# Kernel optimization log

Hardware: AMD Instinct MI355X
Metric: run time of the kernel (lower is better)

The kernel has to match this reference:

```python
import jax, jax.numpy as jnp
import numpy as np

V, E, HS, HD = 32000, 64, 128, 128
S, T = 128, 48


def gru_cell(x, h, Wih, Whh, bih, bhh):
    # torch nn.GRU cell: gates stacked as [r, z, n]
    gi = x @ Wih.T + bih
    gh = h @ Whh.T + bhh
    ir, iz, inn = jnp.split(gi, 3, axis=-1)
    hr, hz, hn = jnp.split(gh, 3, axis=-1)
    r = jax.nn.sigmoid(ir + hr)
    z = jax.nn.sigmoid(iz + hz)
    n = jnp.tanh(inn + r * hn)
    return (1.0 - z) * n + z * h


def setup_inputs() -> dict:
    key = jax.random.key(0)
    ks = jax.random.split(key, 16)
    sc = 0.05
    inp = {
        'document': jax.random.randint(ks[0], (S, T), 0, V, dtype=jnp.int64),
        'enc_emb': jax.random.normal(ks[1], (V, E), jnp.float32) * sc,
        'enc_Wih': jax.random.normal(ks[2], (3 * HS, E), jnp.float32) * sc,
        'enc_Whh': jax.random.normal(ks[3], (3 * HS, HS), jnp.float32) * sc,
        'enc_bih': jax.random.normal(ks[4], (3 * HS,), jnp.float32) * sc,
        'enc_bhh': jax.random.normal(ks[5], (3 * HS,), jnp.float32) * sc,
        'doc_Wih': jax.random.normal(ks[6], (3 * HD, HS), jnp.float32) * sc,
        'doc_Whh': jax.random.normal(ks[7], (3 * HD, HD), jnp.float32) * sc,
        'doc_bih': jax.random.normal(ks[8], (3 * HD,), jnp.float32) * sc,
        'doc_bhh': jax.random.normal(ks[9], (3 * HD,), jnp.float32) * sc,
        'dec_emb': jax.random.normal(ks[10], (V, E), jnp.float32) * sc,
        'dec_Wih': jax.random.normal(ks[11], (3 * HS, E + HD), jnp.float32) * sc,
        'dec_Whh': jax.random.normal(ks[12], (3 * HS, HS), jnp.float32) * sc,
        'dec_bih': jax.random.normal(ks[13], (3 * HS,), jnp.float32) * sc,
        'dec_bhh': jax.random.normal(ks[14], (3 * HS,), jnp.float32) * sc,
        'fc_W': jax.random.normal(ks[15], (V, HS), jnp.float32) * sc,
        'fc_b': jnp.zeros((V,), jnp.float32),
    }
    return inp


def reference(document, enc_emb, enc_Wih, enc_Whh, enc_bih, enc_bhh,
              doc_Wih, doc_Whh, doc_bih, doc_bhh,
              dec_emb, dec_Wih, dec_Whh, dec_bih, dec_bhh, fc_W, fc_b):
    s, t = document.shape
    # --- sentence encoder: GRU over tokens, batch = sentences ---
    x = enc_emb[document]                       # [S, T, E]
    def enc_step(h, xt):
        return gru_cell(xt, h, enc_Wih, enc_Whh, enc_bih, enc_bhh), None
    h0 = jnp.zeros((s, HS), enc_emb.dtype)
    sent_vec, _ = jax.lax.scan(enc_step, h0, jnp.swapaxes(x, 0, 1))  # [S, HS]
    # --- document encoder: GRU over sentence vectors, batch = 1 ---
    def doc_step(h, sv):
        return gru_cell(sv[None, :], h, doc_Wih, doc_Whh, doc_bih, doc_bhh), None
    hd0 = jnp.zeros((1, HD), enc_emb.dtype)
    doc_h, _ = jax.lax.scan(doc_step, hd0, sent_vec)
    doc_vec = doc_h[0]                          # [HD]
    # --- teacher-forced decoder, vectorized over sentences ---
    dec_in = dec_emb[document[:, :-1]]          # [S, T-1, E]
    ctx = jnp.broadcast_to(doc_vec, (s, t - 1, HD))
    xs = jnp.swapaxes(jnp.concatenate([dec_in, ctx], axis=-1), 0, 1)  # [T-1, S, E+HD]
    def dec_step(h, xt):
        h2 = gru_cell(xt, h, dec_Wih, dec_Whh, dec_bih, dec_bhh)
        logits = h2 @ fc_W.T + fc_b
        return h2, logits
    _, logits = jax.lax.scan(dec_step, sent_vec, xs)  # [T-1, S, V]
    targets = document[:, 1:].T                 # [T-1, S]
    logp = jax.nn.log_softmax(logits, axis=-1)
    ll = jnp.take_along_axis(logp, targets[..., None], axis=-1)[..., 0]
    # per-sentence mean over steps, then mean over sentences == global mean
    return -jnp.mean(ll)
```

## Files before the change

kernel.cpp:

```cpp
#include <hip/hip_runtime.h>

typedef unsigned short ushort_t;
typedef short bf16x8 __attribute__((ext_vector_type(8)));
typedef float f32x4 __attribute__((ext_vector_type(4)));
typedef unsigned int u32x4 __attribute__((ext_vector_type(4)));
typedef _Float16 half2t __attribute__((ext_vector_type(2)));

#define LOG2E 1.4426950408889634f
#define LN2   0.6931471805599453f

__device__ __forceinline__ float bf2f(ushort_t u) {
    union { unsigned int i; float f; } v; v.i = ((unsigned int)u) << 16; return v.f;
}
__device__ __forceinline__ ushort_t f2bf(float f) {
    union { float f; unsigned int i; } v; v.f = f;
    unsigned int u = v.i;
    unsigned int r = (u + 0x7FFFu + ((u >> 16) & 1u)) >> 16;
    return (ushort_t)r;
}
__device__ __forceinline__ float hsum4(f32x4 v) { return (v[0] + v[1]) + (v[2] + v[3]); }
__device__ __forceinline__ float frcp(float x) { return __builtin_amdgcn_rcpf(x); }
__device__ __forceinline__ float fsig(float x) { return frcp(1.f + __expf(-x)); }
__device__ __forceinline__ float ftanh(float x) { return 1.f - 2.f * frcp(1.f + __expf(2.f * x)); }
__device__ __forceinline__ int hpad(int e) { return e + ((e >> 4) << 2); }
__device__ __forceinline__ float dot2(unsigned int w, unsigned int h, float acc) {
    union { unsigned int u; half2t h2; } a, b;
    a.u = w; b.u = h;
    return __builtin_amdgcn_fdot2(a.h2, b.h2, acc, false);
}
__device__ __forceinline__ float dpp_xor1_add(float x) {
    int m = __builtin_amdgcn_update_dpp(0, __builtin_bit_cast(int, x), 0xB1, 0xF, 0xF, true);
    return x + __builtin_bit_cast(float, m);
}
__device__ __forceinline__ float dpp_xor2_add(float x) {
    int m = __builtin_amdgcn_update_dpp(0, __builtin_bit_cast(int, x), 0x4E, 0xF, 0xF, true);
    return x + __builtin_bit_cast(float, m);
}
__device__ __forceinline__ ushort_t f2h(float f) {
    union { _Float16 h; ushort_t s; } c; c.h = (_Float16)f; return c.s;
}

__global__ __launch_bounds__(768, 1) void k_encoder(
    const int* __restrict__ doc, const float* __restrict__ emb,
    const float* __restrict__ Wih, const float* __restrict__ Whh,
    const float* __restrict__ bih, const float* __restrict__ bhh,
    float* __restrict__ sent) {
    int s = blockIdx.x, t = threadIdx.x;
    int half = t & 1, j = t >> 1;
    __shared__ float xs[80], hs[160];
    __shared__ float gi[384], gh[384];
    __shared__ int toks[48];
    f32x4 wih[8], whh[16];
#pragma unroll
    for (int k = 0; k < 8; k++) wih[k] = *(const f32x4*)(Wih + j * 64 + half * 32 + k * 4);
#pragma unroll
    for (int k = 0; k < 16; k++) whh[k] = *(const f32x4*)(Whh + j * 128 + half * 64 + k * 4);
    float bi = bih[j], bh = bhh[j];
    if (t < 48) toks[t] = doc[s * 48 + t];
    if (t < 128) hs[hpad(t)] = 0.f;
    __syncthreads();
    if (t < 64) xs[hpad(t)] = emb[(size_t)toks[0] * 64 + t];
    __syncthreads();
    const float* xb = xs + half * 40;
    const float* hb = hs + half * 80;
    for (int tt = 0; tt < 48; tt++) {
        float xnext = (t < 64 && tt + 1 < 48) ? emb[(size_t)toks[tt + 1] * 64 + t] : 0.f;
        f32x4 a0 = {0,0,0,0}, b0 = {0,0,0,0}, b1 = {0,0,0,0};
#pragma unroll
        for (int k = 0; k < 8; k++) a0 += wih[k] * (*(const f32x4*)(xb + k * 4 + (k >> 2) * 4));
#pragma unroll
        for (int k = 0; k < 16; k += 2) {
            b0 += whh[k] * (*(const f32x4*)(hb + k * 4 + (k >> 2) * 4));
            b1 += whh[k + 1] * (*(const f32x4*)(hb + (k + 1) * 4 + ((k + 1) >> 2) * 4));
        }
        float a = hsum4(a0), b = hsum4(b0 + b1);
        a = dpp_xor1_add(a); b = dpp_xor1_add(b);
        if (half == 0) { gi[j] = a + bi; gh[j] = b + bh; }
        __syncthreads();
        if (t < 128) {
            float r = fsig(gi[t] + gh[t]);
            float z = fsig(gi[t + 128] + gh[t + 128]);
            float n = ftanh(gi[t + 256] + r * gh[t + 256]);
            hs[hpad(t)] = (1.f - z) * n + z * hs[hpad(t)];
        }
        if (t < 64 && tt + 1 < 48) xs[hpad(t)] = xnext;
        __syncthreads();
    }
    if (t < 128) sent[s * 128 + t] = hs[hpad(t)];
}

__global__ void k_doc_gi(const float* __restrict__ sv, const float* __restrict__ Wih,
                         const float* __restrict__ bih, float* __restrict__ gidoc,
                         const float* __restrict__ Whh, ushort_t* __restrict__ wdoc) {
    int bid = blockIdx.x, j = threadIdx.x;
    if (bid >= 128) {
        int i = (bid - 128) * 384 + j;
        if (i < 12288) {
            f32x4 v = ((const f32x4*)Whh)[i];
            union { ushort_t u[4]; unsigned long long q; } p;
            p.u[0] = f2h(v[0]); p.u[1] = f2h(v[1]); p.u[2] = f2h(v[2]); p.u[3] = f2h(v[3]);
            ((unsigned long long*)wdoc)[i] = p.q;
        }
        return;
    }
    __shared__ f32x4 v4[32];
    if (j < 128) ((float*)v4)[j] = sv[bid * 128 + j];
    __syncthreads();
    f32x4 a0 = {0,0,0,0}, a1 = {0,0,0,0};
#pragma unroll
    for (int k = 0; k < 32; k += 2) {
        a0 += *(const f32x4*)(Wih + j * 128 + k * 4) * v4[k];
        a1 += *(const f32x4*)(Wih + j * 128 + (k + 1) * 4) * v4[k + 1];
    }
    gidoc[bid * 384 + j] = bih[j] + hsum4(a0 + a1);
}

__global__ __launch_bounds__(512, 1) __attribute__((amdgpu_waves_per_eu(1, 2)))
void k_mid(
    const float* __restrict__ gidoc, const ushort_t* __restrict__ wdoc,
    const float* __restrict__ dbhh, float* __restrict__ dvec,
    const int* __restrict__ doc, const float* __restrict__ demb,
    const float* __restrict__ dWih, float* __restrict__ gidec,
    const float* __restrict__ fcW, ushort_t* __restrict__ fcWb,
    const float* __restrict__ fcb, float* __restrict__ fcbs) {
    int bid = blockIdx.x, t = threadIdx.x;

    if (bid == 0) {
        int q = t & 3, e = t >> 2;
        __shared__ unsigned int hpk[2][64];
        u32x4 wr4[4], wz4[4], wn4[4];
        const ushort_t* wbase = wdoc + e * 128 + q * 32;
#pragma unroll
        for (int k = 0; k < 4; k++) {
            wr4[k] = *(const u32x4*)(wbase + k * 8);
            wz4[k] = *(const u32x4*)(wbase + 128 * 128 + k * 8);
            wn4[k] = *(const u32x4*)(wbase + 256 * 128 + k * 8);
        }
        float biasr = dbhh[e], biasz = dbhh[128 + e], biasn = dbhh[256 + e];
        float cr = gidoc[e], cz = gidoc[128 + e], cn = gidoc[256 + e];
        if (t < 64) hpk[0][t] = 0u;
        float he = 0.f;
        __syncthreads();
        for (int i = 0; i < 128; i++) {
            float nr = 0.f, nz = 0.f, nn = 0.f;
            if (i + 1 < 128) {
                const float* g = gidoc + (i + 1) * 384;
                nr = g[e]; nz = g[128 + e]; nn = g[256 + e];
            }
            const unsigned int* hp = &hpk[i & 1][q * 16];
            u32x4 hv[4];
            hv[0] = *(const u32x4*)(hp);
            hv[1] = *(const u32x4*)(hp + 4);
            hv[2] = *(const u32x4*)(hp + 8);
            hv[3] = *(const u32x4*)(hp + 12);
            float ra0 = 0.f, ra1 = 0.f, za0 = 0.f, za1 = 0.f, na0 = 0.f, na1 = 0.f;
#pragma unroll
            for (int k = 0; k < 4; k++) {
                u32x4 h4 = hv[k];
                ra0 = dot2(wr4[k][0], h4[0], ra0); ra1 = dot2(wr4[k][1], h4[1], ra1);
                ra0 = dot2(wr4[k][2], h4[2], ra0); ra1 = dot2(wr4[k][3], h4[3], ra1);
                za0 = dot2(wz4[k][0], h4[0], za0); za1 = dot2(wz4[k][1], h4[1], za1);
                za0 = dot2(wz4[k][2], h4[2], za0); za1 = dot2(wz4[k][3], h4[3], za1);
                na0 = dot2(wn4[k][0], h4[0], na0); na1 = dot2(wn4[k][1], h4[1], na1);
                na0 = dot2(wn4[k][2], h4[2], na0); na1 = dot2(wn4[k][3], h4[3], na1);
            }
            float rp = ra0 + ra1, zp = za0 + za1, np = na0 + na1;
            rp = dpp_xor2_add(dpp_xor1_add(rp));
            zp = dpp_xor2_add(dpp_xor1_add(zp));
            np = dpp_xor2_add(dpp_xor1_add(np));
            float r = fsig(cr + rp + biasr);
            float z = fsig(cz + zp + biasz);
            float n = ftanh(cn + r * (np + biasn));
            he = (1.f - z) * n + z * he;
            if (q == 0) ((ushort_t*)&hpk[(i & 1) ^ 1][0])[e] = f2h(he);
            __syncthreads();
            cr = nr; cz = nz; cn = nn;
        }
        if (q == 0) dvec[e] = he;
        return;
    }

    if (bid <= 128) {
        int s = bid - 1;
        __shared__ float xs[80];
        __shared__ int toks[48];
        if (t < 47) toks[t] = doc[s * 48 + t];
        __syncthreads();
        if (t < 64) xs[hpad(t)] = demb[(size_t)toks[0] * 64 + t];
        __syncthreads();
        f32x4 wih[16];
        if (t < 384) {
#pragma unroll
            for (int k = 0; k < 16; k++) wih[k] = *(const f32x4*)(dWih + t * 192 + k * 4);
        }
        for (int tt = 0; tt < 47; tt++) {
            float xnext = (t < 64 && tt + 1 < 47) ? demb[(size_t)toks[tt + 1] * 64 + t] : 0.f;
            if (t < 384) {
                f32x4 a0 = {0,0,0,0}, a1 = {0,0,0,0};
#pragma unroll
                for (int k = 0; k < 16; k += 2) {
                    a0 += wih[k] * (*(const f32x4*)(xs + k * 4 + (k >> 2) * 4));
                    a1 += wih[k + 1] * (*(const f32x4*)(xs + (k + 1) * 4 + ((k + 1) >> 2) * 4));
                }
                gidec[(tt * 128 + s) * 384 + t] = hsum4(a0 + a1);
            }
            __syncthreads();
            if (t < 64 && tt + 1 < 47) xs[hpad(t)] = xnext;
            __syncthreads();
        }
        return;
    }

    int i = (bid - 129) * 512 + t;
    if (i < 1024000) {
        f32x4 v = ((const f32x4*)fcW)[i];
        union { ushort_t u[4]; unsigned long long qq; } p;
        p.u[0] = f2bf(v[0] * LOG2E); p.u[1] = f2bf(v[1] * LOG2E);
        p.u[2] = f2bf(v[2] * LOG2E); p.u[3] = f2bf(v[3] * LOG2E);
        ((unsigned long long*)fcWb)[i] = p.qq;
    } else if (i < 1024000 + 8000) {
        int k = i - 1024000;
        f32x4 b = ((const f32x4*)fcb)[k];
        ((f32x4*)fcbs)[k] = b * LOG2E;
    }
}

__global__ void k_gctx(const float* __restrict__ Wih, const float* __restrict__ bih,
                       const float* __restrict__ dvec, float* __restrict__ gctx) {
    int j = threadIdx.x;
    __shared__ f32x4 v4[32];
    if (j < 128) ((float*)v4)[j] = dvec[j];
    __syncthreads();
    f32x4 a0 = {0,0,0,0}, a1 = {0,0,0,0};
#pragma unroll
    for (int k = 0; k < 32; k += 2) {
        a0 += *(const f32x4*)(Wih + j * 192 + 64 + k * 4) * v4[k];
        a1 += *(const f32x4*)(Wih + j * 192 + 64 + (k + 1) * 4) * v4[k + 1];
    }
    gctx[j] = bih[j] + hsum4(a0 + a1);
}

__global__ __launch_bounds__(768, 1) void k_dec_seq(
    const float* __restrict__ gidec, const float* __restrict__ Whh,
    const float* __restrict__ bhh, const float* __restrict__ sent,
    const float* __restrict__ gctx, ushort_t* __restrict__ h2b) {
    int s = blockIdx.x, t = threadIdx.x, half = t & 1, j = t >> 1;
    __shared__ float hs[160];
    __shared__ float gi[384], gh[384];
    f32x4 whh[16];
#pragma unroll
    for (int k = 0; k < 16; k++) whh[k] = *(const f32x4*)(Whh + j * 128 + half * 64 + k * 4);
    float bh = bhh[j];
    float g_me = gctx[j];
    if (t < 128) hs[hpad(t)] = sent[s * 128 + t];
    float gval = (half == 0) ? (gidec[s * 384 + j] + g_me) : 0.f;
    __syncthreads();
    const float* hb = hs + half * 80;
    for (int i = 0; i < 47; i++) {
        float gnext = (half == 0 && i + 1 < 47) ? (gidec[((i + 1) * 128 + s) * 384 + j] + g_me) : 0.f;
        f32x4 b0 = {0,0,0,0}, b1 = {0,0,0,0};
#pragma unroll
        for (int k = 0; k < 16; k += 2) {
            b0 += whh[k] * (*(const f32x4*)(hb + k * 4 + (k >> 2) * 4));
            b1 += whh[k + 1] * (*(const f32x4*)(hb + (k + 1) * 4 + ((k + 1) >> 2) * 4));
        }
        float b = hsum4(b0 + b1);
        b = dpp_xor1_add(b);
        if (half == 0) { gh[j] = b + bh; gi[j] = gval; }
        __syncthreads();
        if (t < 128) {
            float r = fsig(gi[t] + gh[t]);
            float z = fsig(gi[t + 128] + gh[t + 128]);
            float n = ftanh(gi[t + 256] + r * gh[t + 256]);
            float hn = (1.f - z) * n + z * hs[hpad(t)];
            hs[hpad(t)] = hn;
            h2b[(i * 128 + s) * 128 + t] = f2bf(hn);
        }
        __syncthreads();
        gval = gnext;
    }
}

__global__ void k_tl(const int* __restrict__ doc, const ushort_t* __restrict__ h2b,
                     const ushort_t* __restrict__ wb, const float* __restrict__ fcb,
                     float* __restrict__ tl) {
    int r = blockIdx.x * 4 + (threadIdx.x >> 6);
    int lane = threadIdx.x & 63;
    int s = r & 127, t = r >> 7;
    int tok = doc[s * 48 + t + 1];
    const ushort_t* hp = h2b + r * 128;
    const ushort_t* wp = wb + tok * 128;
    float acc = bf2f(hp[lane]) * bf2f(wp[lane]) + bf2f(hp[lane + 64]) * bf2f(wp[lane + 64]);
#pragma unroll
    for (int m = 32; m >= 1; m >>= 1) acc += __shfl_xor(acc, m);
    if (lane == 0) tl[r] = acc * LN2 + fcb[tok];
}

#define LSE_VC 10
#define LSE_NC 3200
#define LSE_NPAIR 25
__global__ __launch_bounds__(512, 2) void k_lse(
    const ushort_t* __restrict__ h2b, const ushort_t* __restrict__ wb,
    const float* __restrict__ fcbs, float* __restrict__ parts) {
    int rb = blockIdx.x / LSE_VC;
    int vc = blockIdx.x % LSE_VC;
    int t = threadIdx.x;
    int wave = t >> 6, lane = t & 63;
    int rg = wave >> 1, cg = wave & 1;
    int q = lane >> 4, l15 = lane & 15;

    __shared__ __align__(16) char ldsB[65536];

    int row0 = rb * 128 + rg * 32;
    bf16x8 a[2][4];
    const ushort_t* ap = h2b + (size_t)(row0 + l15) * 128 + q * 8;
#pragma unroll
    for (int m = 0; m < 2; m++)
#pragma unroll
        for (int c = 0; c < 4; c++) a[m][c] = *(const bf16x8*)(ap + m * 2048 + c * 32);

    const char* wbB = (const char*)wb;
    int so = ((t >> 4) << 8) + (((t & 15) ^ ((t >> 4) & 15)) << 4);
    char* dst1 = ldsB + wave * 1024;

#define LSE_STAGE(buf, cb) do { \
    const char* g_ = wbB + (size_t)(cb) * 256 + so; \
    char* d_ = dst1 + (buf) * 16384; \
    __builtin_amdgcn_global_load_lds((const __attribute__((address_space(1))) unsigned int*)(g_), \
                                     (__attribute__((address_space(3))) unsigned int*)(d_), 16, 0, 0); \
    __builtin_amdgcn_global_load_lds((const __attribute__((address_space(1))) unsigned int*)(g_ + 8192), \
                                     (__attribute__((address_space(3))) unsigned int*)(d_ + 8192), 16, 0, 0); \
} while (0)

    int ra[2][4];
#pragma unroll
    for (int c2 = 0; c2 < 2; c2++)
#pragma unroll
        for (int c = 0; c < 4; c++)
            ra[c2][c] = (cg * 32 + c2 * 16 + l15) * 256 + (((q + 4 * c) ^ l15) << 4);

    int cb0 = vc * LSE_NC;
    f32x4 se[2] = {{0,0,0,0},{0,0,0,0}};

    LSE_STAGE(0, cb0);
    LSE_STAGE(1, cb0 + 64);
    __syncthreads();
    int cur = 0;
    for (int it = 0; it < LSE_NPAIR; ++it) {
        if (it + 1 < LSE_NPAIR) {
            LSE_STAGE(2 * (cur ^ 1),     cb0 + (2 * it + 2) * 64);
            LSE_STAGE(2 * (cur ^ 1) + 1, cb0 + (2 * it + 3) * 64);
        }
        int colg = cb0 + 2 * it * 64 + cg * 32 + l15;
        float bA0 = fcbs[colg],      bA1 = fcbs[colg + 16];
        float bB0 = fcbs[colg + 64], bB1 = fcbs[colg + 80];
#pragma unroll
        for (int half = 0; half < 2; half++) {
            const char* bb = ldsB + (size_t)(2 * cur + half) * 16384;
            float bs0 = half ? bB0 : bA0;
            float bs1 = half ? bB1 : bA1;
            f32x4 acc[2][2] = {{{0,0,0,0},{0,0,0,0}},{{0,0,0,0},{0,0,0,0}}};
#pragma unroll
            for (int c = 0; c < 4; c++) {
                bf16x8 b0 = *(const bf16x8*)(bb + ra[0][c]);
                bf16x8 b1 = *(const bf16x8*)(bb + ra[1][c]);
                acc[0][0] = __builtin_amdgcn_mfma_f32_16x16x32_bf16(a[0][c], b0, acc[0][0], 0, 0, 0);
                acc[1][0] = __builtin_amdgcn_mfma_f32_16x16x32_bf16(a[1][c], b0, acc[1][0], 0, 0, 0);
                acc[0][1] = __builtin_amdgcn_mfma_f32_16x16x32_bf16(a[0][c], b1, acc[0][1], 0, 0, 0);
                acc[1][1] = __builtin_amdgcn_mfma_f32_16x16x32_bf16(a[1][c], b1, acc[1][1], 0, 0, 0);
            }
#pragma unroll
            for (int m = 0; m < 2; m++) {
#pragma unroll
                for (int r = 0; r < 4; r++)
                    se[m][r] += __builtin_amdgcn_exp2f(acc[m][0][r] + bs0)
                              + __builtin_amdgcn_exp2f(acc[m][1][r] + bs1);
            }
        }
        __syncthreads();
        cur ^= 1;
    }

#pragma unroll
    for (int m = 0; m < 2; m++) {
        f32x4 v = se[m];
#pragma unroll
        for (int d = 1; d < 16; d <<= 1) {
            v[0] += __shfl_xor(v[0], d);
            v[1] += __shfl_xor(v[1], d);
            v[2] += __shfl_xor(v[2], d);
            v[3] += __shfl_xor(v[3], d);
        }
        if (l15 == 0) {
            float* p = parts + (size_t)(vc * 2 + cg) * 6016 + row0 + m * 16 + q * 4;
            p[0] = v[0]; p[1] = v[1]; p[2] = v[2]; p[3] = v[3];
        }
    }
}

__global__ void k_final1(const float* __restrict__ parts, const float* __restrict__ tl,
                         float* __restrict__ rowloss) {
    int r = blockIdx.x * 128 + threadIdx.x;
    float tot = 0.f;
#pragma unroll 4
    for (int c = 0; c < 20; c++) tot += parts[(size_t)c * 6016 + r];
    rowloss[r] = logf(tot) - tl[r];
}

__global__ void k_final2(const float* __restrict__ rowloss, float* __restrict__ out) {
    __shared__ float red[512];
    int tid = threadIdx.x;
    float acc = 0.f;
    for (int r = tid; r < 6016; r += 512) acc += rowloss[r];
    red[tid] = acc;
    __syncthreads();
    for (int s = 256; s > 0; s >>= 1) {
        if (tid < s) red[tid] += red[tid + s];
        __syncthreads();
    }
    if (tid == 0) out[0] = red[0] / 6016.f;
}

extern "C" void kernel_launch(void* const* d_in, const int* in_sizes, int n_in,
                              void* d_out, int out_size, void* d_ws, size_t ws_size,
                              hipStream_t stream) {
    const int* doc = (const int*)d_in[0];
    const float* enc_emb = (const float*)d_in[1];
    const float* enc_Wih = (const float*)d_in[2];
    const float* enc_Whh = (const float*)d_in[3];
    const float* enc_bih = (const float*)d_in[4];
    const float* enc_bhh = (const float*)d_in[5];
    const float* doc_Wih = (const float*)d_in[6];
    const float* doc_Whh = (const float*)d_in[7];
    const float* doc_bih = (const float*)d_in[8];
    const float* doc_bhh = (const float*)d_in[9];
    const float* dec_emb = (const float*)d_in[10];
    const float* dec_Wih = (const float*)d_in[11];
    const float* dec_Whh = (const float*)d_in[12];
    const float* dec_bih = (const float*)d_in[13];
    const float* dec_bhh = (const float*)d_in[14];
    const float* fc_W = (const float*)d_in[15];
    const float* fc_b = (const float*)d_in[16];

    char* ws = (char*)d_ws;
    ushort_t* fcWb = (ushort_t*)(ws + 0);
    float* sent    = (float*)(ws + 8192000);
    float* dvec    = (float*)(ws + 8257536);
    float* gidoc   = (float*)(ws + 8258048);
    float* gidec   = (float*)(ws + 8456192);
    ushort_t* h2b  = (ushort_t*)(ws + 17696768);
    float* tl      = (float*)(ws + 19236864);
    float* parts   = (float*)(ws + 19260928);
    float* rowloss = (float*)(ws + 20223488);
    ushort_t* wdoc = (ushort_t*)(ws + 20247552);
    float* fcbs    = (float*)(ws + 20345856);
    float* gctx    = (float*)(ws + 20473856);
    float* out = (float*)d_out;

    k_encoder<<<128, 768, 0, stream>>>(doc, enc_emb, enc_Wih, enc_Whh, enc_bih, enc_bhh, sent);
    k_doc_gi<<<160, 384, 0, stream>>>(sent, doc_Wih, doc_bih, gidoc, doc_Whh, wdoc);
    k_mid<<<1 + 128 + 2016, 512, 0, stream>>>(gidoc, wdoc, doc_bhh, dvec,
                                              doc, dec_emb, dec_Wih, gidec,
                                              fc_W, fcWb, fc_b, fcbs);
    k_gctx<<<1, 384, 0, stream>>>(dec_Wih, dec_bih, dvec, gctx);
    k_dec_seq<<<128, 768, 0, stream>>>(gidec, dec_Whh, dec_bhh, sent, gctx, h2b);
    k_tl<<<1504, 256, 0, stream>>>(doc, h2b, fcWb, fc_b, tl);
    k_lse<<<47 * LSE_VC, 512, 0, stream>>>(h2b, fcWb, fcbs, parts);
    k_final1<<<47, 128, 0, stream>>>(parts, tl, rowloss);
    k_final2<<<1, 512, 0, stream>>>(rowloss, out);
}
```

Baseline: 252.4 us.

## Use fp16 packed dot2 for encoder and decoder recurrent matvecs

Adds a prep kernel that converts the encoder input/hidden weights and the decoder hidden weights to fp16, alongside the existing doc weight conversion that used to live in k_doc_gi. The encoder and decoder recurrences now keep packed fp16 weights in registers and the hidden and input vectors as fp16 in shared memory, and compute the matvecs with v_dot2 instead of fp32 vector FMAs. Each thread keeps its own hidden element in an fp32 register. The aim is to shorten the serial per-step latency by halving register and LDS traffic and the instruction count. The cost is fp16 rounding of weights and state on every step, an extra kernel launch, and relocated workspace offsets.

```diff
diff --git a/kernel.cpp b/kernel.cpp
--- a/kernel.cpp
+++ b/kernel.cpp
@@ -40,71 +40,85 @@
     union { _Float16 h; ushort_t s; } c; c.h = (_Float16)f; return c.s;
 }
 
+__global__ void k_prep(const float* __restrict__ encWih, const float* __restrict__ encWhh,
+                       const float* __restrict__ decWhh, const float* __restrict__ docWhh,
+                       ushort_t* __restrict__ wencih, ushort_t* __restrict__ wenchh,
+                       ushort_t* __restrict__ wdechh, ushort_t* __restrict__ wdoc) {
+    int i = blockIdx.x * blockDim.x + threadIdx.x;
+    const float* src; ushort_t* dst; int off;
+    if (i < 6144)       { src = encWih; dst = wencih; off = i; }
+    else if (i < 18432) { src = encWhh; dst = wenchh; off = i - 6144; }
+    else if (i < 30720) { src = decWhh; dst = wdechh; off = i - 18432; }
+    else if (i < 43008) { src = docWhh; dst = wdoc;   off = i - 30720; }
+    else return;
+    f32x4 v = ((const f32x4*)src)[off];
+    union { ushort_t u[4]; unsigned long long q; } p;
+    p.u[0] = f2h(v[0]); p.u[1] = f2h(v[1]); p.u[2] = f2h(v[2]); p.u[3] = f2h(v[3]);
+    ((unsigned long long*)dst)[off] = p.q;
+}
+
 __global__ __launch_bounds__(768, 1) void k_encoder(
     const int* __restrict__ doc, const float* __restrict__ emb,
-    const float* __restrict__ Wih, const float* __restrict__ Whh,
+    const ushort_t* __restrict__ wih16, const ushort_t* __restrict__ whh16,
     const float* __restrict__ bih, const float* __restrict__ bhh,
     float* __restrict__ sent) {
     int s = blockIdx.x, t = threadIdx.x;
     int half = t & 1, j = t >> 1;
-    __shared__ float xs[80], hs[160];
+    __shared__ unsigned int xpk[32], hpk_[64];
     __shared__ float gi[384], gh[384];
     __shared__ int toks[48];
-    f32x4 wih[8], whh[16];
-#pragma unroll
-    for (int k = 0; k < 8; k++) wih[k] = *(const f32x4*)(Wih + j * 64 + half * 32 + k * 4);
-#pragma unroll
-    for (int k = 0; k < 16; k++) whh[k] = *(const f32x4*)(Whh + j * 128 + half * 64 + k * 4);
+    u32x4 wi[4], wh[8];
+    const ushort_t* pih = wih16 + j * 64 + half * 32;
+    const ushort_t* phh = whh16 + j * 128 + half * 64;
+#pragma unroll
+    for (int k = 0; k < 4; k++) wi[k] = *(const u32x4*)(pih + k * 8);
+#pragma unroll
+    for (int k = 0; k < 8; k++) wh[k] = *(const u32x4*)(phh + k * 8);
     float bi = bih[j], bh = bhh[j];
     if (t < 48) toks[t] = doc[s * 48 + t];
-    if (t < 128) hs[hpad(t)] = 0.f;
-    __syncthreads();
-    if (t < 64) xs[hpad(t)] = emb[(size_t)toks[0] * 64 + t];
-    __syncthreads();
-    const float* xb = xs + half * 40;
-    const float* hb = hs + half * 80;
+    if (t < 64) hpk_[t] = 0u;
+    __syncthreads();
+    if (t < 64) ((ushort_t*)xpk)[t] = f2h(emb[(size_t)toks[0] * 64 + t]);
+    float h_own = 0.f;
+    __syncthreads();
+    const unsigned int* xb = xpk + half * 16;
+    const unsigned int* hb = hpk_ + half * 32;
     for (int tt = 0; tt < 48; tt++) {
         float xnext = (t < 64 && tt + 1 < 48) ? emb[(size_t)toks[tt + 1] * 64 + t] : 0.f;
-        f32x4 a0 = {0,0,0,0}, b0 = {0,0,0,0}, b1 = {0,0,0,0};
-#pragma unroll
-        for (int k = 0; k < 8; k++) a0 += wih[k] * (*(const f32x4*)(xb + k * 4 + (k >> 2) * 4));
-#pragma unroll
-        for (int k = 0; k < 16; k += 2) {
-            b0 += whh[k] * (*(const f32x4*)(hb + k * 4 + (k >> 2) * 4));
-            b1 += whh[k + 1] * (*(const f32x4*)(hb + (k + 1) * 4 + ((k + 1) >> 2) * 4));
-        }
-        float a = hsum4(a0), b = hsum4(b0 + b1);
-        a = dpp_xor1_add(a); b = dpp_xor1_add(b);
+        float a0 = 0.f, a1 = 0.f, b0 = 0.f, b1 = 0.f;
+#pragma unroll
+        for (int k = 0; k < 4; k++) {
+            u32x4 xv = *(const u32x4*)(xb + k * 4);
+            a0 = dot2(wi[k][0], xv[0], a0); a1 = dot2(wi[k][1], xv[1], a1);
+            a0 = dot2(wi[k][2], xv[2], a0); a1 = dot2(wi[k][3], xv[3], a1);
+        }
+#pragma unroll
+        for (int k = 0; k < 8; k++) {
+            u32x4 hv = *(const u32x4*)(hb + k * 4);
+            b0 = dot2(wh[k][0], hv[0], b0); b1 = dot2(wh[k][1], hv[1], b1);
+            b0 = dot2(wh[k][2], hv[2], b0); b1 = dot2(wh[k][3], hv[3], b1);
+        }
+        float a = dpp_xor1_add(a0 + a1), b = dpp_xor1_add(b0 + b1);
         if (half == 0) { gi[j] = a + bi; gh[j] = b + bh; }
         __syncthreads();
         if (t < 128) {
             float r = fsig(gi[t] + gh[t]);
             float z = fsig(gi[t + 128] + gh[t + 128]);
             float n = ftanh(gi[t + 256] + r * gh[t + 256]);
-            hs[hpad(t)] = (1.f - z) * n + z * hs[hpad(t)];
-        }
-        if (t < 64 && tt + 1 < 48) xs[hpad(t)] = xnext;
-        __syncthreads();
-    }
-    if (t < 128) sent[s * 128 + t] = hs[hpad(t)];
+            h_own = (1.f - z) * n + z * h_own;
+            ((ushort_t*)hpk_)[t] = f2h(h_own);
+        }
+        if (t < 64 && tt + 1 < 48) ((ushort_t*)xpk)[t] = f2h(xnext);
+        __syncthreads();
+    }
+    if (t < 128) sent[s * 128 + t] = h_own;
 }
 
 __global__ void k_doc_gi(const float* __restrict__ sv, const float* __restrict__ Wih,
-                         const float* __restrict__ bih, float* __restrict__ gidoc,
-                         const float* __restrict__ Whh, ushort_t* __restrict__ wdoc) {
-    int bid = blockIdx.x, j = threadIdx.x;
-    if (bid >= 128) {
-        int i = (bid - 128) * 384 + j;
-        if (i < 12288) {
-            f32x4 v = ((const f32x4*)Whh)[i];
-            union { ushort_t u[4]; unsigned long long q; } p;
-            p.u[0] = f2h(v[0]); p.u[1] = f2h(v[1]); p.u[2] = f2h(v[2]); p.u[3] = f2h(v[3]);
-            ((unsigned long long*)wdoc)[i] = p.q;
-        }
-        return;
-    }
+                         const float* __restrict__ bih, float* __restrict__ gidoc) {
+    int i = blockIdx.x, j = threadIdx.x;
     __shared__ f32x4 v4[32];
-    if (j < 128) ((float*)v4)[j] = sv[bid * 128 + j];
+    if (j < 128) ((float*)v4)[j] = sv[i * 128 + j];
     __syncthreads();
     f32x4 a0 = {0,0,0,0}, a1 = {0,0,0,0};
 #pragma unroll
@@ -112,7 +126,7 @@
         a0 += *(const f32x4*)(Wih + j * 128 + k * 4) * v4[k];
         a1 += *(const f32x4*)(Wih + j * 128 + (k + 1) * 4) * v4[k + 1];
     }
-    gidoc[bid * 384 + j] = bih[j] + hsum4(a0 + a1);
+    gidoc[i * 384 + j] = bih[j] + hsum4(a0 + a1);
 }
 
 __global__ __launch_bounds__(512, 1) __attribute__((amdgpu_waves_per_eu(1, 2)))
@@ -241,40 +255,42 @@
 }
 
 __global__ __launch_bounds__(768, 1) void k_dec_seq(
-    const float* __restrict__ gidec, const float* __restrict__ Whh,
+    const float* __restrict__ gidec, const ushort_t* __restrict__ whh16,
     const float* __restrict__ bhh, const float* __restrict__ sent,
     const float* __restrict__ gctx, ushort_t* __restrict__ h2b) {
     int s = blockIdx.x, t = threadIdx.x, half = t & 1, j = t >> 1;
-    __shared__ float hs[160];
+    __shared__ unsigned int hpk_[64];
     __shared__ float gi[384], gh[384];
-    f32x4 whh[16];
-#pragma unroll
-    for (int k = 0; k < 16; k++) whh[k] = *(const f32x4*)(Whh + j * 128 + half * 64 + k * 4);
+    u32x4 wh[8];
+    const ushort_t* phh = whh16 + j * 128 + half * 64;
+#pragma unroll
+    for (int k = 0; k < 8; k++) wh[k] = *(const u32x4*)(phh + k * 8);
     float bh = bhh[j];
     float g_me = gctx[j];
-    if (t < 128) hs[hpad(t)] = sent[s * 128 + t];
+    float h_own = 0.f;
+    if (t < 128) { h_own = sent[s * 128 + t]; ((ushort_t*)hpk_)[t] = f2h(h_own); }
     float gval = (half == 0) ? (gidec[s * 384 + j] + g_me) : 0.f;
     __syncthreads();
-    const float* hb = hs + half * 80;
+    const unsigned int* hb = hpk_ + half * 32;
     for (int i = 0; i < 47; i++) {
         float gnext = (half == 0 && i + 1 < 47) ? (gidec[((i + 1) * 128 + s) * 384 + j] + g_me) : 0.f;
-        f32x4 b0 = {0,0,0,0}, b1 = {0,0,0,0};
-#pragma unroll
-        for (int k = 0; k < 16; k += 2) {
-            b0 += whh[k] * (*(const f32x4*)(hb + k * 4 + (k >> 2) * 4));
-            b1 += whh[k + 1] * (*(const f32x4*)(hb + (k + 1) * 4 + ((k + 1) >> 2) * 4));
-        }
-        float b = hsum4(b0 + b1);
-        b = dpp_xor1_add(b);
+        float b0 = 0.f, b1 = 0.f;
+#pragma unroll
+        for (int k = 0; k < 8; k++) {
+            u32x4 hv = *(const u32x4*)(hb + k * 4);
+            b0 = dot2(wh[k][0], hv[0], b0); b1 = dot2(wh[k][1], hv[1], b1);
+            b0 = dot2(wh[k][2], hv[2], b0); b1 = dot2(wh[k][3], hv[3], b1);
+        }
+        float b = dpp_xor1_add(b0 + b1);
         if (half == 0) { gh[j] = b + bh; gi[j] = gval; }
         __syncthreads();
         if (t < 128) {
             float r = fsig(gi[t] + gh[t]);
             float z = fsig(gi[t + 128] + gh[t + 128]);
             float n = ftanh(gi[t + 256] + r * gh[t + 256]);
-            float hn = (1.f - z) * n + z * hs[hpad(t)];
-            hs[hpad(t)] = hn;
-            h2b[(i * 128 + s) * 128 + t] = f2bf(hn);
+            h_own = (1.f - z) * n + z * h_own;
+            ((ushort_t*)hpk_)[t] = f2h(h_own);
+            h2b[(i * 128 + s) * 128 + t] = f2bf(h_own);
         }
         __syncthreads();
         gval = gnext;
@@ -443,27 +459,32 @@
     const float* fc_b = (const float*)d_in[16];
 
     char* ws = (char*)d_ws;
-    ushort_t* fcWb = (ushort_t*)(ws + 0);
-    float* sent    = (float*)(ws + 8192000);
-    float* dvec    = (float*)(ws + 8257536);
-    float* gidoc   = (float*)(ws + 8258048);
-    float* gidec   = (float*)(ws + 8456192);
-    ushort_t* h2b  = (ushort_t*)(ws + 17696768);
-    float* tl      = (float*)(ws + 19236864);
-    float* parts   = (float*)(ws + 19260928);
-    float* rowloss = (float*)(ws + 20223488);
-    ushort_t* wdoc = (ushort_t*)(ws + 20247552);
-    float* fcbs    = (float*)(ws + 20345856);
-    float* gctx    = (float*)(ws + 20473856);
+    ushort_t* fcWb   = (ushort_t*)(ws + 0);
+    float* sent      = (float*)(ws + 8192000);
+    float* dvec      = (float*)(ws + 8257536);
+    float* gidoc     = (float*)(ws + 8258048);
+    float* gidec     = (float*)(ws + 8456192);
+    ushort_t* h2b    = (ushort_t*)(ws + 17696768);
+    float* tl        = (float*)(ws + 19236864);
+    float* parts     = (float*)(ws + 19260928);
+    float* rowloss   = (float*)(ws + 19742208);
+    ushort_t* wdoc   = (ushort_t*)(ws + 19766272);
+    float* fcbs      = (float*)(ws + 19864576);
+    float* gctx      = (float*)(ws + 19992576);
+    ushort_t* wencih = (ushort_t*)(ws + 19994112);
+    ushort_t* wenchh = (ushort_t*)(ws + 20043264);
+    ushort_t* wdechh = (ushort_t*)(ws + 20141568);
     float* out = (float*)d_out;
 
-    k_encoder<<<128, 768, 0, stream>>>(doc, enc_emb, enc_Wih, enc_Whh, enc_bih, enc_bhh, sent);
-    k_doc_gi<<<160, 384, 0, stream>>>(sent, doc_Wih, doc_bih, gidoc, doc_Whh, wdoc);
+    k_prep<<<168, 256, 0, stream>>>(enc_Wih, enc_Whh, dec_Whh, doc_Whh,
+                                    wencih, wenchh, wdechh, wdoc);
+    k_encoder<<<128, 768, 0, stream>>>(doc, enc_emb, wencih, wenchh, enc_bih, enc_bhh, sent);
+    k_doc_gi<<<128, 384, 0, stream>>>(sent, doc_Wih, doc_bih, gidoc);
     k_mid<<<1 + 128 + 2016, 512, 0, stream>>>(gidoc, wdoc, doc_bhh, dvec,
                                               doc, dec_emb, dec_Wih, gidec,
                                               fc_W, fcWb, fc_b, fcbs);
     k_gctx<<<1, 384, 0, stream>>>(dec_Wih, dec_bih, dvec, gctx);
-    k_dec_seq<<<128, 768, 0, stream>>>(gidec, dec_Whh, dec_bhh, sent, gctx, h2b);
+    k_dec_seq<<<128, 768, 0, stream>>>(gidec, wdechh, dec_bhh, sent, gctx, h2b);
     k_tl<<<1504, 256, 0, stream>>>(doc, h2b, fcWb, fc_b, tl);
     k_lse<<<47 * LSE_VC, 512, 0, stream>>>(h2b, fcWb, fcbs, parts);
     k_final1<<<47, 128, 0, stream>>>(parts, tl, rowloss);
```

Measured after the change: 231.1 us. 1.09x faster.
